# Performance work log

Measured on AMD Instinct MI355X. Metric: run time of the kernel, lower is better.

Reference implementation:

```python
import jax, jax.numpy as jnp
import numpy as np

N_NODES = 50000
N_EDGES = 600000
N_SUB = 20000
E_SUB = 120000
D = 128

def setup_inputs() -> dict:
    key = jax.random.key(0)
    ks = jax.random.split(key, 16)
    s = 1.0 / np.sqrt(D)
    inp = {
        "x": jax.random.normal(ks[0], (N_NODES, D), dtype=jnp.float32),
        "Wm": jax.random.normal(ks[1], (D, D), dtype=jnp.float32) * s,
        "bm": jnp.zeros((D,), dtype=jnp.float32),
        "Wn2s0": jax.random.normal(ks[2], (D, D), dtype=jnp.float32) * s,
        "bn2s0": jnp.zeros((D,), dtype=jnp.float32),
        "Ws2n0": jax.random.normal(ks[3], (D, D), dtype=jnp.float32) * s,
        "bs2n0": jnp.zeros((D,), dtype=jnp.float32),
        "Wn2s1": jax.random.normal(ks[4], (D, D), dtype=jnp.float32) * s,
        "bn2s1": jnp.zeros((D,), dtype=jnp.float32),
        "Ws2n1": jax.random.normal(ks[5], (D, D), dtype=jnp.float32) * s,
        "bs2n1": jnp.zeros((D,), dtype=jnp.float32),
        "neighbor_edge_index": jax.random.randint(ks[6], (2, N_EDGES), 0, N_NODES, dtype=jnp.int64),
        "sub_row0": jax.random.randint(ks[7], (E_SUB,), 0, N_NODES, dtype=jnp.int64),
        "sub_col0": jax.random.randint(ks[8], (E_SUB,), 0, N_SUB, dtype=jnp.int64),
        "sub_row1": jax.random.randint(ks[9], (E_SUB,), 0, N_NODES, dtype=jnp.int64),
        "sub_col1": jax.random.randint(ks[10], (E_SUB,), 0, N_SUB, dtype=jnp.int64),
    }
    return inp


def _level(x, row, col, Wn2s, bn2s, Ws2n, bs2n):
    # node -> substructure: gather node feats, sum-reduce into substructures
    sub_x = jax.ops.segment_sum(x[row], col, num_segments=N_SUB)  # [n_sub, D]
    sub_x = sub_x @ Wn2s + bn2s
    # substructure -> node: gather substructure feats, sum-reduce back to nodes
    msg = jax.ops.segment_sum(sub_x[col], row, num_segments=N_NODES)  # [N, D]
    msg = msg @ Ws2n + bs2n
    return x + msg


def reference(x, Wm, bm, Wn2s0, bn2s0, Ws2n0, bs2n0, Wn2s1, bn2s1, Ws2n1, bs2n1,
              neighbor_edge_index, sub_row0, sub_col0, sub_row1, sub_col1):
    src, dst = neighbor_edge_index[0], neighbor_edge_index[1]
    # message_neighbor: GIN-like sum aggregation + Linear + ReLU
    agg = jax.ops.segment_sum(x[src], dst, num_segments=N_NODES)
    x = jax.nn.relu((x + agg) @ Wm + bm)
    # substructure levels (gather -> scatter-sum -> Linear -> gather -> scatter-sum -> Linear -> residual)
    x = _level(x, sub_row0, sub_col0, Wn2s0, bn2s0, Ws2n0, bs2n0)
    x = _level(x, sub_row1, sub_col1, Wn2s1, bn2s1, Ws2n1, bs2n1)
    return x
```

## Files before the change

### kernel.cpp

```cpp
#include <hip/hip_runtime.h>
#include <hip/hip_fp16.h>

#define D 128
#define NN 50000
#define NS 20000
#define NNP 50048
#define NSP 20032
#define L_TOT (3 * NN + 2 * NS)
#define LDA 136

#define NB_BKT 188
#define CBUF_SLOTS 1296384
#define HIST_CHUNK 4096
#define HIST_BLOCKS 264

typedef short s16x8 __attribute__((ext_vector_type(8)));
typedef float f32x4 __attribute__((ext_vector_type(4)));

__device__ __forceinline__ float b2f(unsigned int u) {
    u <<= 16;
    float f; __builtin_memcpy(&f, &u, 4);
    return f;
}
__device__ __forceinline__ unsigned short f2b(float f) {
    unsigned int u; __builtin_memcpy(&u, &f, 4);
    u += 0x7fffu + ((u >> 16) & 1u);
    return (unsigned short)(u >> 16);
}
__device__ __forceinline__ void acc8(float* a, uint4 v) {
    a[0] += b2f(v.x & 0xffffu); a[1] += b2f(v.x >> 16);
    a[2] += b2f(v.y & 0xffffu); a[3] += b2f(v.y >> 16);
    a[4] += b2f(v.z & 0xffffu); a[5] += b2f(v.z >> 16);
    a[6] += b2f(v.w & 0xffffu); a[7] += b2f(v.w >> 16);
}

__device__ __forceinline__ unsigned int f2h8(float f) {
    __half h = __float2half(f);
    unsigned short us; __builtin_memcpy(&us, &h, 2);
    unsigned int v = us;
    v += 0x7fu + ((v >> 8) & 1u);
    return (v >> 8) & 0xffu;
}
__device__ __forceinline__ void acch4(float* a, unsigned int w) {
    unsigned int h01 = __builtin_amdgcn_perm(w, w, 0x010c000cu);
    unsigned int h23 = __builtin_amdgcn_perm(w, w, 0x030c020cu);
    __half2 p; float2 f;
    __builtin_memcpy(&p, &h01, 4); f = __half22float2(p); a[0] += f.x; a[1] += f.y;
    __builtin_memcpy(&p, &h23, 4); f = __half22float2(p); a[2] += f.x; a[3] += f.y;
}
__device__ __forceinline__ void acch16(float* a, uint4 v) {
    acch4(a + 0,  v.x); acch4(a + 4,  v.y);
    acch4(a + 8,  v.z); acch4(a + 12, v.w);
}

__device__ __forceinline__ void bkt_geom(int b, int& capOff, int& cap) {
    if (b < 98)       { capOff = b * 7168;                  cap = 7168; }
    else if (b < 118) { capOff = 702464  + (b - 98)  * 7168; cap = 7168; }
    else if (b < 143) { capOff = 845824  + (b - 118) * 6144; cap = 6144; }
    else if (b < 163) { capOff = 999424  + (b - 143) * 7168; cap = 7168; }
    else              { capOff = 1142784 + (b - 163) * 6144; cap = 6144; }
}

#define NX4 (NN * D / 4)
#define NW  (5 * 16384)
#define PREP_N (NX4 + NW)
#define PREP_BLOCKS ((PREP_N + 255) / 256)

struct PrepHistArgs {
    const float* x; unsigned short* xb; unsigned int* xb8;
    const float* w[5]; unsigned short* wt[5];
    const int* s0; const int* s1; const int* s2; const int* s3; const int* s4;
    const int* v0; const int* v1; const int* v2; const int* v3; const int* v4;
    unsigned int* coarse;
    int* cursor;
    int nE, eS, tot;
};
__global__ __launch_bounds__(256) void preph_k(PrepHistArgs p)
{
    __shared__ int cnt_l[NB_BKT];
    __shared__ int gb_l[NB_BKT];
    __shared__ int rk_l[NB_BKT];

    int bid = blockIdx.x;
    int tid = threadIdx.x;
    if (bid < PREP_BLOCKS) {
        int i = bid * 256 + tid;
        if (i < NX4) {
            float4 v = ((const float4*)p.x)[i];
            ushort4 o;
            o.x = f2b(v.x); o.y = f2b(v.y); o.z = f2b(v.z); o.w = f2b(v.w);
            ((ushort4*)p.xb)[i] = o;
            p.xb8[i] = f2h8(v.x) | (f2h8(v.y) << 8) | (f2h8(v.z) << 16) | (f2h8(v.w) << 24);
            return;
        }
        i -= NX4;
        if (i < NW) {
            int wi = i >> 14;
            int r  = i & 16383;
            int k = r >> 7, n = r & 127;
            p.wt[wi][n * 128 + k] = f2b(p.w[wi][k * 128 + n]);
        }
        return;
    }

    int e0 = (bid - PREP_BLOCKS) * HIST_CHUNK;
    unsigned int pk[16];
    int bk[16];
    #pragma unroll
    for (int i = 0; i < 16; ++i) {
        int e = e0 + i * 256 + tid;
        bk[i] = -1;
        if (e < p.tot) {
            int seg, val, region;
            if (e < p.nE) { seg = p.s0[e]; val = p.v0[e]; region = 0; }
            else {
                int r = e - p.nE;
                if      (r <     p.eS) { seg = p.s1[r];            val = p.v1[r];            region = 1; }
                else if (r < 2 * p.eS) { seg = p.s2[r - p.eS];     val = p.v2[r - p.eS];     region = 2; }
                else if (r < 3 * p.eS) { seg = p.s3[r - 2 * p.eS]; val = p.v3[r - 2 * p.eS]; region = 3; }
                else                   { seg = p.s4[r - 3 * p.eS]; val = p.v4[r - 3 * p.eS]; region = 4; }
            }
            int shift, bktBase;
            if      (region == 0) { shift = 9;  bktBase = 0;   }
            else if (region == 1) { shift = 10; bktBase = 98;  }
            else if (region == 2) { shift = 11; bktBase = 118; }
            else if (region == 3) { shift = 10; bktBase = 143; }
            else                  { shift = 11; bktBase = 163; }
            int lb = seg & ((1 << shift) - 1);
            bk[i] = bktBase + (seg >> shift);
            pk[i] = ((unsigned int)lb << 16) | (unsigned int)(val & 0xffff);
        }
    }
    if (tid < NB_BKT) cnt_l[tid] = 0;
    __syncthreads();
    #pragma unroll
    for (int i = 0; i < 16; ++i)
        if (bk[i] >= 0) atomicAdd(&cnt_l[bk[i]], 1);
    __syncthreads();
    if (tid < NB_BKT) {
        int c = cnt_l[tid];
        gb_l[tid] = (c > 0) ? atomicAdd(&p.cursor[tid], c) : 0;
        rk_l[tid] = 0;
    }
    __syncthreads();
    #pragma unroll
    for (int i = 0; i < 16; ++i) {
        if (bk[i] >= 0) {
            int b = bk[i];
            int r = atomicAdd(&rk_l[b], 1);
            int pos = gb_l[b] + r;
            int capOff, cap;
            bkt_geom(b, capOff, cap);
            if (pos < cap) p.coarse[capOff + pos] = pk[i];
        }
    }
}

__global__ __launch_bounds__(256) void fine_k(
    const unsigned int* __restrict__ coarse, const int* __restrict__ cursor,
    int* __restrict__ offsets, unsigned short* __restrict__ perm)
{
    __shared__ int hist[2048];
    __shared__ int cur[2048];
    __shared__ int part[256];

    int b = blockIdx.x;
    int tid = threadIdx.x;

    part[tid] = (tid < NB_BKT) ? cursor[tid] : 0;
    __syncthreads();
    for (int off = 1; off < 256; off <<= 1) {
        int t = (tid >= off) ? part[tid - off] : 0;
        __syncthreads();
        part[tid] += t;
        __syncthreads();
    }
    int permBase = (b > 0) ? part[b - 1] : 0;
    __syncthreads();

    int bIn, shift, regionBins, gBinBase;
    if (b < 98)       { bIn = b;       shift = 9;  regionBins = NN; gBinBase = 0; }
    else if (b < 118) { bIn = b - 98;  shift = 10; regionBins = NS; gBinBase = NN; }
    else if (b < 143) { bIn = b - 118; shift = 11; regionBins = NN; gBinBase = NN + NS; }
    else if (b < 163) { bIn = b - 143; shift = 10; regionBins = NS; gBinBase = 2 * NN + NS; }
    else              { bIn = b - 163; shift = 11; regionBins = NN; gBinBase = 2 * NN + 2 * NS; }
    int BS = 1 << shift;
    int localBinBase = bIn << shift;
    int nb = regionBins - localBinBase; if (nb > BS) nb = BS;
    int g0 = gBinBase + localBinBase;
    int capOff, cap;
    bkt_geom(b, capOff, cap);
    const unsigned int* src = coarse + capOff;
    int cnt = cursor[b]; if (cnt > cap) cnt = cap;

    for (int i = tid; i < 2048; i += 256) hist[i] = 0;
    __syncthreads();
    for (int i = tid; i < cnt; i += 256)
        atomicAdd(&hist[src[i] >> 16], 1);
    __syncthreads();

    int base8 = tid * 8;
    int loc[8]; int s = 0;
    #pragma unroll
    for (int j = 0; j < 8; ++j) { loc[j] = hist[base8 + j]; s += loc[j]; }
    part[tid] = s;
    __syncthreads();
    for (int off = 1; off < 256; off <<= 1) {
        int t = (tid >= off) ? part[tid - off] : 0;
        __syncthreads();
        part[tid] += t;
        __syncthreads();
    }
    int run = (tid > 0) ? part[tid - 1] : 0;
    #pragma unroll
    for (int j = 0; j < 8; ++j) { cur[base8 + j] = run; run += loc[j]; }
    __syncthreads();

    for (int i = tid; i < nb; i += 256)
        offsets[g0 + i + 1] = permBase + cur[i] + hist[i];
    __syncthreads();

    for (int i = tid; i < cnt; i += 256) {
        unsigned int w = src[i];
        int lb = (int)(w >> 16);
        int pos = atomicAdd(&cur[lb], 1);
        perm[permBase + pos] = (unsigned short)(w & 0xffffu);
    }
    if (b == 0 && tid == 0) offsets[0] = 0;
}

__global__ __launch_bounds__(512, 4) void gg_k(
    const unsigned short* __restrict__ feat, const unsigned int* __restrict__ feat8,
    const int* __restrict__ offsets, const unsigned short* __restrict__ perm,
    const unsigned short* __restrict__ addend,
    const unsigned short* __restrict__ Wt, const float* __restrict__ bias,
    const unsigned short* __restrict__ Rb,
    float* __restrict__ outF, unsigned short* __restrict__ outB,
    int M, int relu)
{
    __shared__ unsigned short a_lds[64 * LDA];

    const int tid = threadIdx.x;
    const int r0  = blockIdx.x * 64;

    if (feat8) {
        const uint4* f8 = (const uint4*)feat8;
        const int g  = tid >> 3;
        const int l8 = tid & 7;
        const int s  = r0 + g;
        float a[16], b[16];
        #pragma unroll
        for (int i = 0; i < 16; ++i) { a[i] = 0.f; b[i] = 0.f; }
        if (s < M) {
            if (addend) {
                const uint4* ad = (const uint4*)(addend + (size_t)s * D);
                uint4 v0 = ad[l8 * 2], v1 = ad[l8 * 2 + 1];
                acc8(a, v0); acc8(a + 8, v1);
            }
            int beg = offsets[s], end = offsets[s + 1];
            int j = beg;
            for (; j + 7 < end; j += 8) {
                int e0 = perm[j],     e1 = perm[j + 1], e2 = perm[j + 2], e3 = perm[j + 3];
                int e4 = perm[j + 4], e5 = perm[j + 5], e6 = perm[j + 6], e7 = perm[j + 7];
                uint4 v0 = f8[(size_t)e0 * 8 + l8];
                uint4 v1 = f8[(size_t)e1 * 8 + l8];
                uint4 v2 = f8[(size_t)e2 * 8 + l8];
                uint4 v3 = f8[(size_t)e3 * 8 + l8];
                uint4 v4 = f8[(size_t)e4 * 8 + l8];
                uint4 v5 = f8[(size_t)e5 * 8 + l8];
                uint4 v6 = f8[(size_t)e6 * 8 + l8];
                uint4 v7 = f8[(size_t)e7 * 8 + l8];
                acch16(a, v0); acch16(b, v1); acch16(a, v2); acch16(b, v3);
                acch16(a, v4); acch16(b, v5); acch16(a, v6); acch16(b, v7);
            }
            for (; j + 3 < end; j += 4) {
                int e0 = perm[j], e1 = perm[j + 1], e2 = perm[j + 2], e3 = perm[j + 3];
                uint4 v0 = f8[(size_t)e0 * 8 + l8];
                uint4 v1 = f8[(size_t)e1 * 8 + l8];
                uint4 v2 = f8[(size_t)e2 * 8 + l8];
                uint4 v3 = f8[(size_t)e3 * 8 + l8];
                acch16(a, v0); acch16(b, v1); acch16(a, v2); acch16(b, v3);
            }
            for (; j < end; ++j)
                acch16(a, f8[(size_t)perm[j] * 8 + l8]);
            #pragma unroll
            for (int i = 0; i < 16; ++i) a[i] += b[i];
        }
        uint4 o0, o1;
        o0.x = (unsigned int)f2b(a[0])  | ((unsigned int)f2b(a[1])  << 16);
        o0.y = (unsigned int)f2b(a[2])  | ((unsigned int)f2b(a[3])  << 16);
        o0.z = (unsigned int)f2b(a[4])  | ((unsigned int)f2b(a[5])  << 16);
        o0.w = (unsigned int)f2b(a[6])  | ((unsigned int)f2b(a[7])  << 16);
        o1.x = (unsigned int)f2b(a[8])  | ((unsigned int)f2b(a[9])  << 16);
        o1.y = (unsigned int)f2b(a[10]) | ((unsigned int)f2b(a[11]) << 16);
        o1.z = (unsigned int)f2b(a[12]) | ((unsigned int)f2b(a[13]) << 16);
        o1.w = (unsigned int)f2b(a[14]) | ((unsigned int)f2b(a[15]) << 16);
        *((uint4*)&a_lds[g * LDA + l8 * 16])     = o0;
        *((uint4*)&a_lds[g * LDA + l8 * 16 + 8]) = o1;
    } else {
        const uint4* f4 = (const uint4*)feat;
        const int lane16 = tid & 15;
        #pragma unroll
        for (int p = 0; p < 2; ++p) {
            int rloc = p * 32 + (tid >> 4);
            int s = r0 + rloc;
            float a[8] = {0.f, 0.f, 0.f, 0.f, 0.f, 0.f, 0.f, 0.f};
            if (s < M) {
                float b[8] = {0.f, 0.f, 0.f, 0.f, 0.f, 0.f, 0.f, 0.f};
                if (addend) {
                    uint4 v = ((const uint4*)(addend + (size_t)s * D))[lane16];
                    acc8(a, v);
                }
                int beg = offsets[s], end = offsets[s + 1];
                int j = beg;
                for (; j + 7 < end; j += 8) {
                    int e0 = perm[j],     e1 = perm[j + 1], e2 = perm[j + 2], e3 = perm[j + 3];
                    int e4 = perm[j + 4], e5 = perm[j + 5], e6 = perm[j + 6], e7 = perm[j + 7];
                    uint4 v0 = f4[(size_t)e0 * 16 + lane16];
                    uint4 v1 = f4[(size_t)e1 * 16 + lane16];
                    uint4 v2 = f4[(size_t)e2 * 16 + lane16];
                    uint4 v3 = f4[(size_t)e3 * 16 + lane16];
                    uint4 v4 = f4[(size_t)e4 * 16 + lane16];
                    uint4 v5 = f4[(size_t)e5 * 16 + lane16];
                    uint4 v6 = f4[(size_t)e6 * 16 + lane16];
                    uint4 v7 = f4[(size_t)e7 * 16 + lane16];
                    acc8(a, v0); acc8(b, v1); acc8(a, v2); acc8(b, v3);
                    acc8(a, v4); acc8(b, v5); acc8(a, v6); acc8(b, v7);
                }
                for (; j + 3 < end; j += 4) {
                    int e0 = perm[j], e1 = perm[j + 1], e2 = perm[j + 2], e3 = perm[j + 3];
                    uint4 v0 = f4[(size_t)e0 * 16 + lane16];
                    uint4 v1 = f4[(size_t)e1 * 16 + lane16];
                    uint4 v2 = f4[(size_t)e2 * 16 + lane16];
                    uint4 v3 = f4[(size_t)e3 * 16 + lane16];
                    acc8(a, v0); acc8(b, v1); acc8(a, v2); acc8(b, v3);
                }
                for (; j < end; ++j)
                    acc8(a, f4[(size_t)perm[j] * 16 + lane16]);
                #pragma unroll
                for (int i = 0; i < 8; ++i) a[i] += b[i];
            }
            uint4 o;
            o.x = (unsigned int)f2b(a[0]) | ((unsigned int)f2b(a[1]) << 16);
            o.y = (unsigned int)f2b(a[2]) | ((unsigned int)f2b(a[3]) << 16);
            o.z = (unsigned int)f2b(a[4]) | ((unsigned int)f2b(a[5]) << 16);
            o.w = (unsigned int)f2b(a[6]) | ((unsigned int)f2b(a[7]) << 16);
            *((uint4*)&a_lds[rloc * LDA + lane16 * 8]) = o;
        }
    }
    __syncthreads();

    const int lane = tid & 63;
    const int w    = tid >> 6;
    const int wr   = w & 3;
    const int wc   = w >> 2;
    const int ln   = lane & 15;
    const int quad = lane >> 4;

    s16x8 af[4];
    const unsigned short* arow = &a_lds[(wr * 16 + ln) * LDA + quad * 8];
    #pragma unroll
    for (int kc = 0; kc < 4; ++kc)
        af[kc] = *((const s16x8*)(arow + kc * 32));

    const int rbase = r0 + wr * 16 + quad * 4;
    const s16x8* wt8 = (const s16x8*)Wt;

    #pragma unroll
    for (int nt = 0; nt < 4; ++nt) {
        f32x4 acc = {0.f, 0.f, 0.f, 0.f};
        int col = wc * 64 + nt * 16 + ln;
        const s16x8* brow = wt8 + col * 16 + quad;
        #pragma unroll
        for (int kc = 0; kc < 4; ++kc) {
            s16x8 bf = brow[kc * 4];
            acc = __builtin_amdgcn_mfma_f32_16x16x32_bf16(af[kc], bf, acc, 0, 0, 0);
        }
        float bc = bias[col];
        #pragma unroll
        for (int r = 0; r < 4; ++r) {
            int row = rbase + r;
            if (row < M) {
                float v = acc[r] + bc;
                size_t gi = (size_t)row * D + col;
                if (Rb) v += b2f((unsigned int)Rb[gi]);
                if (relu) v = fmaxf(v, 0.f);
                if (outF) outF[gi] = v;
                if (outB) outB[gi] = f2b(v);
            }
        }
    }
}

extern "C" void kernel_launch(void* const* d_in, const int* in_sizes, int n_in,
                              void* d_out, int out_size, void* d_ws, size_t ws_size,
                              hipStream_t stream)
{
    const float* x     = (const float*)d_in[0];
    const float* Wm    = (const float*)d_in[1];
    const float* bm    = (const float*)d_in[2];
    const float* Wn2s0 = (const float*)d_in[3];
    const float* bn2s0 = (const float*)d_in[4];
    const float* Ws2n0 = (const float*)d_in[5];
    const float* bs2n0 = (const float*)d_in[6];
    const float* Wn2s1 = (const float*)d_in[7];
    const float* bn2s1 = (const float*)d_in[8];
    const float* Ws2n1 = (const float*)d_in[9];
    const float* bs2n1 = (const float*)d_in[10];
    const int* nei  = (const int*)d_in[11];
    const int* row0 = (const int*)d_in[12];
    const int* col0 = (const int*)d_in[13];
    const int* row1 = (const int*)d_in[14];
    const int* col1 = (const int*)d_in[15];

    const int N_E = in_sizes[11] / 2;
    const int E_S = in_sizes[12];
    const int TOT_E = N_E + 4 * E_S;

    const int* src = nei;
    const int* dst = nei + N_E;

    float* out = (float*)d_out;

    unsigned short* xb   = (unsigned short*)d_ws;
    unsigned short* hbf  = xb  + (size_t)NNP * D;
    unsigned short* subb = hbf + (size_t)NNP * D;
    unsigned short* wtb  = subb + (size_t)NSP * D;
    unsigned short* perm = wtb + 5 * 16384;
    int* ip = (int*)(perm + ((TOT_E + 1) & ~1));
    unsigned int* xb8    = (unsigned int*)ip; ip += NX4;
    unsigned int* coarse = (unsigned int*)ip; ip += CBUF_SLOTS;
    int* cursor     = ip;  ip += 192;
    int* offsets    = ip;  ip += L_TOT + 1;

    unsigned short* wt0 = wtb;
    unsigned short* wt1 = wtb + 16384;
    unsigned short* wt2 = wtb + 2 * 16384;
    unsigned short* wt3 = wtb + 3 * 16384;
    unsigned short* wt4 = wtb + 4 * 16384;

    const int* offB  = offsets;
    const int* off0c = offsets + NN;
    const int* off0r = offsets + NN + NS;
    const int* off1c = offsets + 2 * NN + NS;
    const int* off1r = offsets + 2 * NN + 2 * NS;

    dim3 blk(256);
    dim3 blkG(512);
    dim3 gGemmN(NNP / 64);
    dim3 gGemmS(NSP / 64);
    dim3 gPrepH(PREP_BLOCKS + HIST_BLOCKS);

    hipMemsetAsync(cursor, 0, 192 * sizeof(int), stream);
    PrepHistArgs pa;
    pa.x = x; pa.xb = xb; pa.xb8 = xb8;
    pa.w[0] = Wm;  pa.w[1] = Wn2s0; pa.w[2] = Ws2n0; pa.w[3] = Wn2s1; pa.w[4] = Ws2n1;
    pa.wt[0] = wt0; pa.wt[1] = wt1; pa.wt[2] = wt2; pa.wt[3] = wt3; pa.wt[4] = wt4;
    pa.s0 = dst;  pa.s1 = col0; pa.s2 = row0; pa.s3 = col1; pa.s4 = row1;
    pa.v0 = src;  pa.v1 = row0; pa.v2 = col0; pa.v3 = row1; pa.v4 = col1;
    pa.coarse = coarse; pa.cursor = cursor;
    pa.nE = N_E; pa.eS = E_S; pa.tot = TOT_E;
    preph_k<<<gPrepH, blk, 0, stream>>>(pa);

    fine_k<<<NB_BKT, blk, 0, stream>>>(coarse, cursor, offsets, perm);

    gg_k<<<gGemmN, blkG, 0, stream>>>(xb, xb8, offB, perm, xb, wt0, bm,
                                      nullptr, nullptr, hbf, NN, 1);

    gg_k<<<gGemmS, blkG, 0, stream>>>(hbf, nullptr, off0c, perm, nullptr, wt1, bn2s0,
                                      nullptr, nullptr, subb, NS, 0);
    gg_k<<<gGemmN, blkG, 0, stream>>>(subb, nullptr, off0r, perm, nullptr, wt2, bs2n0,
                                      hbf, nullptr, xb, NN, 0);

    gg_k<<<gGemmS, blkG, 0, stream>>>(xb, nullptr, off1c, perm, nullptr, wt3, bn2s1,
                                      nullptr, nullptr, subb, NS, 0);
    gg_k<<<gGemmN, blkG, 0, stream>>>(subb, nullptr, off1r, perm, nullptr, wt4, bs2n1,
                                      xb, out, nullptr, NN, 0);
}
```

Before: 300.1 us.

## Stage bucket scatter in LDS and specialize gather-GEMM kernels via templates

Measured after the change: 283.3 us. 1.06x faster.

```diff
diff --git a/kernel.cpp b/kernel.cpp
--- a/kernel.cpp
+++ b/kernel.cpp
@@ -80,6 +80,10 @@
     __shared__ int cnt_l[NB_BKT];
     __shared__ int gb_l[NB_BKT];
     __shared__ int rk_l[NB_BKT];
+    __shared__ int ls_l[NB_BKT];
+    __shared__ int part[256];
+    __shared__ unsigned int   st_pk[HIST_CHUNK];
+    __shared__ unsigned short st_bk[HIST_CHUNK];
 
     int bid = blockIdx.x;
     int tid = threadIdx.x;
@@ -137,22 +141,39 @@
     for (int i = 0; i < 16; ++i)
         if (bk[i] >= 0) atomicAdd(&cnt_l[bk[i]], 1);
     __syncthreads();
+    part[tid] = (tid < NB_BKT) ? cnt_l[tid] : 0;
+    __syncthreads();
+    for (int off = 1; off < 256; off <<= 1) {
+        int t = (tid >= off) ? part[tid - off] : 0;
+        __syncthreads();
+        part[tid] += t;
+        __syncthreads();
+    }
+    if (tid < NB_BKT) ls_l[tid] = part[tid] - cnt_l[tid];
     if (tid < NB_BKT) {
         int c = cnt_l[tid];
         gb_l[tid] = (c > 0) ? atomicAdd(&p.cursor[tid], c) : 0;
         rk_l[tid] = 0;
     }
     __syncthreads();
+    int btot = part[NB_BKT - 1];
     #pragma unroll
     for (int i = 0; i < 16; ++i) {
         if (bk[i] >= 0) {
             int b = bk[i];
             int r = atomicAdd(&rk_l[b], 1);
-            int pos = gb_l[b] + r;
-            int capOff, cap;
-            bkt_geom(b, capOff, cap);
-            if (pos < cap) p.coarse[capOff + pos] = pk[i];
-        }
+            int lp = ls_l[b] + r;
+            st_pk[lp] = pk[i];
+            st_bk[lp] = (unsigned short)b;
+        }
+    }
+    __syncthreads();
+    for (int i = tid; i < btot; i += 256) {
+        int b = st_bk[i];
+        int pos = gb_l[b] + (i - ls_l[b]);
+        int capOff, cap;
+        bkt_geom(b, capOff, cap);
+        if (pos < cap) p.coarse[capOff + pos] = st_pk[i];
     }
 }
 
@@ -229,21 +250,21 @@
     if (b == 0 && tid == 0) offsets[0] = 0;
 }
 
-__global__ __launch_bounds__(512, 4) void gg_k(
+template<bool FP8, bool HAS_ADD, bool HAS_RB, bool OUT_F, bool OUT_B, bool RELU>
+__device__ __forceinline__ void gg_body(
     const unsigned short* __restrict__ feat, const unsigned int* __restrict__ feat8,
     const int* __restrict__ offsets, const unsigned short* __restrict__ perm,
     const unsigned short* __restrict__ addend,
     const unsigned short* __restrict__ Wt, const float* __restrict__ bias,
     const unsigned short* __restrict__ Rb,
-    float* __restrict__ outF, unsigned short* __restrict__ outB,
-    int M, int relu)
+    float* __restrict__ outF, unsigned short* __restrict__ outB, int M)
 {
     __shared__ unsigned short a_lds[64 * LDA];
 
     const int tid = threadIdx.x;
     const int r0  = blockIdx.x * 64;
 
-    if (feat8) {
+    if (FP8) {
         const uint4* f8 = (const uint4*)feat8;
         const int g  = tid >> 3;
         const int l8 = tid & 7;
@@ -252,7 +273,7 @@
         #pragma unroll
         for (int i = 0; i < 16; ++i) { a[i] = 0.f; b[i] = 0.f; }
         if (s < M) {
-            if (addend) {
+            if (HAS_ADD) {
                 const uint4* ad = (const uint4*)(addend + (size_t)s * D);
                 uint4 v0 = ad[l8 * 2], v1 = ad[l8 * 2 + 1];
                 acc8(a, v0); acc8(a + 8, v1);
@@ -307,7 +328,7 @@
             float a[8] = {0.f, 0.f, 0.f, 0.f, 0.f, 0.f, 0.f, 0.f};
             if (s < M) {
                 float b[8] = {0.f, 0.f, 0.f, 0.f, 0.f, 0.f, 0.f, 0.f};
-                if (addend) {
+                if (HAS_ADD) {
                     uint4 v = ((const uint4*)(addend + (size_t)s * D))[lane16];
                     acc8(a, v);
                 }
@@ -383,13 +404,52 @@
             if (row < M) {
                 float v = acc[r] + bc;
                 size_t gi = (size_t)row * D + col;
-                if (Rb) v += b2f((unsigned int)Rb[gi]);
-                if (relu) v = fmaxf(v, 0.f);
-                if (outF) outF[gi] = v;
-                if (outB) outB[gi] = f2b(v);
+                if (HAS_RB) v += b2f((unsigned int)Rb[gi]);
+                if (RELU) v = fmaxf(v, 0.f);
+                if (OUT_F) outF[gi] = v;
+                if (OUT_B) outB[gi] = f2b(v);
             }
         }
     }
+}
+
+__global__ __launch_bounds__(512, 4) void gg1_k(
+    const unsigned short* feat, const unsigned int* feat8, const int* offsets,
+    const unsigned short* perm, const unsigned short* addend,
+    const unsigned short* Wt, const float* bias, unsigned short* outB, int M)
+{
+    gg_body<true, true, false, false, true, true>(feat, feat8, offsets, perm,
+        addend, Wt, bias, nullptr, nullptr, outB, M);
+}
+__global__ __launch_bounds__(512, 4) void gg2_k(
+    const unsigned short* feat, const int* offsets, const unsigned short* perm,
+    const unsigned short* Wt, const float* bias, unsigned short* outB, int M)
+{
+    gg_body<false, false, false, false, true, false>(feat, nullptr, offsets, perm,
+        nullptr, Wt, bias, nullptr, nullptr, outB, M);
+}
+__global__ __launch_bounds__(512, 4) void gg4_k(
+    const unsigned short* feat, const int* offsets, const unsigned short* perm,
+    const unsigned short* Wt, const float* bias, unsigned short* outB, int M)
+{
+    gg_body<false, false, false, false, true, false>(feat, nullptr, offsets, perm,
+        nullptr, Wt, bias, nullptr, nullptr, outB, M);
+}
+__global__ __launch_bounds__(512, 4) void gg3_k(
+    const unsigned short* feat, const int* offsets, const unsigned short* perm,
+    const unsigned short* Wt, const float* bias, const unsigned short* Rb,
+    unsigned short* outB, int M)
+{
+    gg_body<false, false, true, false, true, false>(feat, nullptr, offsets, perm,
+        nullptr, Wt, bias, Rb, nullptr, outB, M);
+}
+__global__ __launch_bounds__(512, 4) void gg5_k(
+    const unsigned short* feat, const int* offsets, const unsigned short* perm,
+    const unsigned short* Wt, const float* bias, const unsigned short* Rb,
+    float* outF, int M)
+{
+    gg_body<false, false, true, true, false, false>(feat, nullptr, offsets, perm,
+        nullptr, Wt, bias, Rb, outF, nullptr, M);
 }
 
 extern "C" void kernel_launch(void* const* d_in, const int* in_sizes, int n_in,
@@ -464,16 +524,11 @@
 
     fine_k<<<NB_BKT, blk, 0, stream>>>(coarse, cursor, offsets, perm);
 
-    gg_k<<<gGemmN, blkG, 0, stream>>>(xb, xb8, offB, perm, xb, wt0, bm,
-                                      nullptr, nullptr, hbf, NN, 1);
-
-    gg_k<<<gGemmS, blkG, 0, stream>>>(hbf, nullptr, off0c, perm, nullptr, wt1, bn2s0,
-                                      nullptr, nullptr, subb, NS, 0);
-    gg_k<<<gGemmN, blkG, 0, stream>>>(subb, nullptr, off0r, perm, nullptr, wt2, bs2n0,
-                                      hbf, nullptr, xb, NN, 0);
-
-    gg_k<<<gGemmS, blkG, 0, stream>>>(xb, nullptr, off1c, perm, nullptr, wt3, bn2s1,
-                                      nullptr, nullptr, subb, NS, 0);
-    gg_k<<<gGemmN, blkG, 0, stream>>>(subb, nullptr, off1r, perm, nullptr, wt4, bs2n1,
-                                      xb, out, nullptr, NN, 0);
-}
+    gg1_k<<<gGemmN, blkG, 0, stream>>>(xb, xb8, offB, perm, xb, wt0, bm, hbf, NN);
+
+    gg2_k<<<gGemmS, blkG, 0, stream>>>(hbf, off0c, perm, wt1, bn2s0, subb, NS);
+    gg3_k<<<gGemmN, blkG, 0, stream>>>(subb, off0r, perm, wt2, bs2n0, hbf, xb, NN);
+
+    gg4_k<<<gGemmS, blkG, 0, stream>>>(xb, off1c, perm, wt3, bn2s1, subb, NS);
+    gg5_k<<<gGemmN, blkG, 0, stream>>>(subb, off1r, perm, wt4, bs2n1, xb, out, NN);
+}
```
